# Kernel tuning notes

Measured on AMD Instinct MI355X. Metric: run time of the kernel, lower is better.

Reference implementation:

```python
import jax, jax.numpy as jnp
import numpy as np

B, N, DIM = 1, 4096, 1024
HEADS, DIM_HEAD = 12, 8
POST_LOG_SCALE = 1.0
SCALE = DIM_HEAD ** -0.5


def setup_inputs() -> dict:
    key = jax.random.key(0)
    kx, kw = jax.random.split(key)
    x = jax.random.normal(kx, (B, N, DIM), dtype=jnp.float32)
    # torch nn.Linear(dim, heads*dim_head*2, bias=False) weight: [2*heads*dim_head, dim]
    W = jax.random.normal(kw, (2 * HEADS * DIM_HEAD, DIM), dtype=jnp.float32) * (DIM ** -0.5)
    return {"x": x, "W": W}


def reference(x, W):
    b, n, _ = x.shape
    # linear: x @ W^T -> [b, n, 2*h*d]; rearrange '(qk h d) -> qk b h n d'
    proj = jnp.einsum('bnc,oc->bno', x, W)
    proj = proj.reshape(b, n, 2, HEADS, DIM_HEAD)
    q = jnp.transpose(proj[:, :, 0], (0, 2, 1, 3))  # [b, h, n, d]
    k = jnp.transpose(proj[:, :, 1], (0, 2, 1, 3))  # [b, h, n, d]
    # small-d QK matmul -> [b, h, n, n]
    gates = jnp.einsum('bhid,bhjd->bhij', q, k) * SCALE
    gates = jax.nn.log_sigmoid(gates) * POST_LOG_SCALE
    # causal_mask = triu(ones, diagonal=0); masked_fill -> zero on/above diagonal
    i = jnp.arange(n)[:, None]
    j = jnp.arange(n)[None, :]
    keep = j < i  # strictly lower-triangular entries survive
    gates = jnp.where(keep, gates, 0.0)
    # flip-cumsum-flip == reverse cumulative sum along last axis
    gates = jax.lax.cumsum(gates, axis=3, reverse=True)
    return gates
```

## Files before the change

kernel.cpp:

```cpp
#include <hip/hip_runtime.h>

#define NTOK 4096
#define DIMC 1024
#define HEADS 12
#define DH 8
#define QSCALE 0.35355339059327373f
#define LOG2E  1.4426950408889634f
#define LN2    0.6931471805599453f
#define QPRE   (QSCALE * LOG2E)

typedef float f4 __attribute__((ext_vector_type(4)));
typedef float f2 __attribute__((ext_vector_type(2)));

#define KOFF (HEADS * NTOK * DH)

__global__ __launch_bounds__(256) void k1_proj(const float* __restrict__ x,
                                               const float* __restrict__ W,
                                               float* __restrict__ qk) {
    __shared__ float xs[8 * 1028];
    const int t = threadIdx.x;
    const int row0 = blockIdx.x * 8;

    const f4* x4 = (const f4*)(x + (size_t)row0 * DIMC);
    #pragma unroll
    for (int i = 0; i < 8; ++i) {
        int f = t + i * 256;
        int r = f >> 8;
        int c4 = f & 255;
        f4 v = x4[f];
        *(f4*)(&xs[r * 1028 + c4 * 4]) = v;
    }
    __syncthreads();

    const int g  = t >> 2;
    const int rg = t & 3;

    f2 acc[2][3];
    #pragma unroll
    for (int a = 0; a < 2; ++a)
        #pragma unroll
        for (int m = 0; m < 3; ++m) acc[a][m] = (f2)(0.f);

    const float* w0 = W + (size_t)(3 * g) * DIMC;
    #pragma unroll 2
    for (int c = 0; c < DIMC; c += 4) {
        f4 w[3];
        #pragma unroll
        for (int m = 0; m < 3; ++m)
            w[m] = *(const f4*)(w0 + (size_t)m * DIMC + c);
        #pragma unroll
        for (int a = 0; a < 2; ++a) {
            f4 xv = *(const f4*)(&xs[(rg * 2 + a) * 1028 + c]);
            #pragma unroll
            for (int m = 0; m < 3; ++m) {
                acc[a][m] = __builtin_elementwise_fma(xv.xy, w[m].xy, acc[a][m]);
                acc[a][m] = __builtin_elementwise_fma(xv.zw, w[m].zw, acc[a][m]);
            }
        }
    }

    #pragma unroll
    for (int m = 0; m < 3; ++m) {
        int o   = 3 * g + m;
        int qkf = (o >= 96) ? 1 : 0;
        int oo  = o - 96 * qkf;
        int h   = oo >> 3;
        int d   = oo & 7;
        #pragma unroll
        for (int a = 0; a < 2; ++a) {
            int n = row0 + rg * 2 + a;
            float v = acc[a][m].x + acc[a][m].y;
            if (!qkf) {
                qk[((size_t)h * NTOK + n) * DH + d] = v * QPRE;
            } else {
                qk[KOFF + (((size_t)h * 16 + (n >> 8)) * DH + d) * 256 + (n & 255)] = v;
            }
        }
    }
}

__device__ __forceinline__ float lsig2(float u) {
    float mn = fminf(u, 0.f);
    float z  = __builtin_amdgcn_exp2f(-fabsf(u));
    return mn - __builtin_amdgcn_logf(1.f + z);
}

__global__ __launch_bounds__(256) void k2_gates(const float* __restrict__ qk,
                                                float* __restrict__ out) {
    const int bid  = blockIdx.x;
    const int h    = bid >> 9;
    const int i0   = (bid & 511) << 3;
    const int t    = threadIdx.x;
    const int lane = t & 63;
    const int wid  = t >> 6;
    const int r0   = i0 + 2 * wid;
    const int r1   = r0 + 1;

    const float* qrow = qk + ((size_t)h * NTOK + r0) * DH;
    f2 q0s[8], q1s[8];
    #pragma unroll
    for (int d = 0; d < 8; ++d) {
        q0s[d] = (f2)(qrow[d]);
        q1s[d] = (f2)(qrow[DH + d]);
    }

    const float* kh = qk + KOFF + (size_t)h * (16 * DH * 256) + 4 * lane;
    float* o0 = out + ((size_t)h * NTOK + r0) * NTOK;
    float* o1 = o0 + NTOK;

    const int cb = r0 >> 8;

    f4 z = (f4)(0.f);
    for (int cc = 15; cc > cb; --cc) {
        const int j0 = cc * 256 + 4 * lane;
        __builtin_nontemporal_store(z, (f4*)(o0 + j0));
        __builtin_nontemporal_store(z, (f4*)(o1 + j0));
    }

    float carry0, carry1;

    {
        const int j0 = cb * 256 + 4 * lane;
        const float* kc = kh + (size_t)cb * (DH * 256);

        f4 kv[8];
        #pragma unroll
        for (int d = 0; d < 8; ++d) kv[d] = *(const f4*)(kc + d * 256);

        f2 A0 = (f2)(0.f), B0 = (f2)(0.f), A1 = (f2)(0.f), B1 = (f2)(0.f);
        #pragma unroll
        for (int d = 0; d < 8; ++d) {
            A0 = __builtin_elementwise_fma(kv[d].xy, q0s[d], A0);
            B0 = __builtin_elementwise_fma(kv[d].zw, q0s[d], B0);
            A1 = __builtin_elementwise_fma(kv[d].xy, q1s[d], A1);
            B1 = __builtin_elementwise_fma(kv[d].zw, q1s[d], B1);
        }

        float g0[4], g1[4];
        g0[0] = (j0 + 0 < r0) ? lsig2(A0.x) : 0.f;
        g0[1] = (j0 + 1 < r0) ? lsig2(A0.y) : 0.f;
        g0[2] = (j0 + 2 < r0) ? lsig2(B0.x) : 0.f;
        g0[3] = (j0 + 3 < r0) ? lsig2(B0.y) : 0.f;
        g1[0] = (j0 + 0 < r1) ? lsig2(A1.x) : 0.f;
        g1[1] = (j0 + 1 < r1) ? lsig2(A1.y) : 0.f;
        g1[2] = (j0 + 2 < r1) ? lsig2(B1.x) : 0.f;
        g1[3] = (j0 + 3 < r1) ? lsig2(B1.y) : 0.f;

        g0[2] += g0[3]; g0[1] += g0[2]; g0[0] += g0[1];
        g1[2] += g1[3]; g1[1] += g1[2]; g1[0] += g1[1];
        const float t0 = g0[0], t1 = g1[0];
        float s0 = t0, s1 = t1;
        #pragma unroll
        for (int off = 1; off < 64; off <<= 1) {
            float v0 = __shfl_down(s0, off, 64);
            float v1 = __shfl_down(s1, off, 64);
            if (lane + off < 64) { s0 += v0; s1 += v1; }
        }
        const float base0 = s0 - t0;
        const float base1 = s1 - t1;
        carry0 = __builtin_amdgcn_readfirstlane(s0);
        carry1 = __builtin_amdgcn_readfirstlane(s1);

        f4 gv0 = {g0[0], g0[1], g0[2], g0[3]};
        f4 gv1 = {g1[0], g1[1], g1[2], g1[3]};
        f4 ov0 = (gv0 + base0) * LN2;
        f4 ov1 = (gv1 + base1) * LN2;
        __builtin_nontemporal_store(ov0, (f4*)(o0 + j0));
        __builtin_nontemporal_store(ov1, (f4*)(o1 + j0));
    }

    for (int cc = cb - 1; cc >= 0; --cc) {
        const int j0 = cc * 256 + 4 * lane;
        const float* kc = kh + (size_t)cc * (DH * 256);

        f4 kv[8];
        #pragma unroll
        for (int d = 0; d < 8; ++d) kv[d] = *(const f4*)(kc + d * 256);

        f2 A0 = (f2)(0.f), B0 = (f2)(0.f), A1 = (f2)(0.f), B1 = (f2)(0.f);
        #pragma unroll
        for (int d = 0; d < 8; ++d) {
            A0 = __builtin_elementwise_fma(kv[d].xy, q0s[d], A0);
            B0 = __builtin_elementwise_fma(kv[d].zw, q0s[d], B0);
            A1 = __builtin_elementwise_fma(kv[d].xy, q1s[d], A1);
            B1 = __builtin_elementwise_fma(kv[d].zw, q1s[d], B1);
        }

        float g0[4], g1[4];
        g0[0] = lsig2(A0.x); g0[1] = lsig2(A0.y);
        g0[2] = lsig2(B0.x); g0[3] = lsig2(B0.y);
        g1[0] = lsig2(A1.x); g1[1] = lsig2(A1.y);
        g1[2] = lsig2(B1.x); g1[3] = lsig2(B1.y);

        g0[2] += g0[3]; g0[1] += g0[2]; g0[0] += g0[1];
        g1[2] += g1[3]; g1[1] += g1[2]; g1[0] += g1[1];
        const float t0 = g0[0], t1 = g1[0];
        float s0 = t0, s1 = t1;
        #pragma unroll
        for (int off = 1; off < 64; off <<= 1) {
            float v0 = __shfl_down(s0, off, 64);
            float v1 = __shfl_down(s1, off, 64);
            if (lane + off < 64) { s0 += v0; s1 += v1; }
        }
        const float base0 = (s0 - t0) + carry0;
        const float base1 = (s1 - t1) + carry1;
        carry0 += __builtin_amdgcn_readfirstlane(s0);
        carry1 += __builtin_amdgcn_readfirstlane(s1);

        f4 gv0 = {g0[0], g0[1], g0[2], g0[3]};
        f4 gv1 = {g1[0], g1[1], g1[2], g1[3]};
        f4 ov0 = (gv0 + base0) * LN2;
        f4 ov1 = (gv1 + base1) * LN2;
        __builtin_nontemporal_store(ov0, (f4*)(o0 + j0));
        __builtin_nontemporal_store(ov1, (f4*)(o1 + j0));
    }
}

extern "C" void kernel_launch(void* const* d_in, const int* in_sizes, int n_in,
                              void* d_out, int out_size, void* d_ws, size_t ws_size,
                              hipStream_t stream) {
    const float* x = (const float*)d_in[0];
    const float* W = (const float*)d_in[1];
    float* out = (float*)d_out;
    float* qk  = (float*)d_ws;

    hipLaunchKernelGGL(k1_proj, dim3(NTOK / 8), dim3(256), 0, stream, x, W, qk);
    hipLaunchKernelGGL(k2_gates, dim3(HEADS * NTOK / 8), dim3(256), 0, stream, qk, out);
}
```

Measured before the change: 203.4 us.

## Split upper-triangle zeroing into separate kernel and prefetch next K chunk

Moves the zero-fill of the upper-triangular output region out of the gates kernel into a dedicated k_zero kernel launched first, using regular (not nontemporal) stores over 64x256 tiles. The gates kernel also software-pipelines K loads, fetching the next chunk's keys while computing log-sigmoid and scan on the current one. This aims to balance per-block work (rows near the top no longer do mostly zero stores) and hide load latency, at the cost of an extra launch and more live registers.

New measurement: 224.9 us. +10.6%, slower.

```diff
diff --git a/kernel.cpp b/kernel.cpp
--- a/kernel.cpp
+++ b/kernel.cpp
@@ -76,6 +76,23 @@
                 qk[KOFF + (((size_t)h * 16 + (n >> 8)) * DH + d) * 256 + (n & 255)] = v;
             }
         }
+    }
+}
+
+__global__ __launch_bounds__(256) void k_zero(float* __restrict__ out) {
+    const int cc = blockIdx.x;
+    const int yb = blockIdx.y;
+    const int h  = blockIdx.z;
+    if (cc <= (yb >> 2)) return;
+    const int t = threadIdx.x;
+    float* base = out + ((size_t)h * NTOK + yb * 64) * NTOK + cc * 256;
+    f4 z = (f4)(0.f);
+    #pragma unroll
+    for (int i = 0; i < 16; ++i) {
+        int p = t + i * 256;
+        int r = p >> 6;
+        int c = p & 63;
+        *(f4*)(base + (size_t)r * NTOK + c * 4) = z;
     }
 }
 
@@ -110,22 +127,17 @@
 
     const int cb = r0 >> 8;
 
-    f4 z = (f4)(0.f);
-    for (int cc = 15; cc > cb; --cc) {
-        const int j0 = cc * 256 + 4 * lane;
-        __builtin_nontemporal_store(z, (f4*)(o0 + j0));
-        __builtin_nontemporal_store(z, (f4*)(o1 + j0));
-    }
-
     float carry0, carry1;
+
+    f4 kv[8];
+    {
+        const float* kc = kh + (size_t)cb * (DH * 256);
+        #pragma unroll
+        for (int d = 0; d < 8; ++d) kv[d] = *(const f4*)(kc + d * 256);
+    }
 
     {
         const int j0 = cb * 256 + 4 * lane;
-        const float* kc = kh + (size_t)cb * (DH * 256);
-
-        f4 kv[8];
-        #pragma unroll
-        for (int d = 0; d < 8; ++d) kv[d] = *(const f4*)(kc + d * 256);
 
         f2 A0 = (f2)(0.f), B0 = (f2)(0.f), A1 = (f2)(0.f), B1 = (f2)(0.f);
         #pragma unroll
@@ -134,6 +146,13 @@
             B0 = __builtin_elementwise_fma(kv[d].zw, q0s[d], B0);
             A1 = __builtin_elementwise_fma(kv[d].xy, q1s[d], A1);
             B1 = __builtin_elementwise_fma(kv[d].zw, q1s[d], B1);
+        }
+
+        {
+            const int cn = (cb > 0) ? (cb - 1) : 0;
+            const float* kn = kh + (size_t)cn * (DH * 256);
+            #pragma unroll
+            for (int d = 0; d < 8; ++d) kv[d] = *(const f4*)(kn + d * 256);
         }
 
         float g0[4], g1[4];
@@ -171,11 +190,6 @@
 
     for (int cc = cb - 1; cc >= 0; --cc) {
         const int j0 = cc * 256 + 4 * lane;
-        const float* kc = kh + (size_t)cc * (DH * 256);
-
-        f4 kv[8];
-        #pragma unroll
-        for (int d = 0; d < 8; ++d) kv[d] = *(const f4*)(kc + d * 256);
 
         f2 A0 = (f2)(0.f), B0 = (f2)(0.f), A1 = (f2)(0.f), B1 = (f2)(0.f);
         #pragma unroll
@@ -184,6 +198,13 @@
             B0 = __builtin_elementwise_fma(kv[d].zw, q0s[d], B0);
             A1 = __builtin_elementwise_fma(kv[d].xy, q1s[d], A1);
             B1 = __builtin_elementwise_fma(kv[d].zw, q1s[d], B1);
+        }
+
+        {
+            const int cn = (cc > 0) ? (cc - 1) : 0;
+            const float* kn = kh + (size_t)cn * (DH * 256);
+            #pragma unroll
+            for (int d = 0; d < 8; ++d) kv[d] = *(const f4*)(kn + d * 256);
         }
 
         float g0[4], g1[4];
@@ -224,6 +245,7 @@
     float* out = (float*)d_out;
     float* qk  = (float*)d_ws;
 
+    hipLaunchKernelGGL(k_zero, dim3(16, 64, 12), dim3(256), 0, stream, out);
     hipLaunchKernelGGL(k1_proj, dim3(NTOK / 8), dim3(256), 0, stream, x, W, qk);
     hipLaunchKernelGGL(k2_gates, dim3(HEADS * NTOK / 8), dim3(256), 0, stream, qk, out);
 }
```
